# Performance work log

Measured on AMD Instinct MI355X. Metric: run time of the kernel, lower is better.

## Reference

```python
import jax, jax.numpy as jnp
import numpy as np

N = 50000          # nodes
E = 400000         # edges (before self loops)
F_IN = 128         # NUM_FEATURES
HID = 32           # hidden_dim
H = 12             # heads
HC = H * HID       # concat dim = 384
CLASSES = 40       # NUM_CLASSES
NEG_SLOPE = 0.2    # PyG GATv2 default


def setup_inputs() -> dict:
    key = jax.random.key(0)
    ks = jax.random.split(key, 16)

    def p(k, shape, fan_in):
        return (jax.random.normal(k, shape, jnp.float32) / np.sqrt(fan_in)).astype(jnp.float32)

    return {
        "x": jax.random.normal(ks[0], (N, F_IN), jnp.float32),
        "edge_index": jax.random.randint(ks[1], (2, E), 0, N, jnp.int32),
        # GATv2 layer 1 (share_weights=False)
        "Wl1": p(ks[2], (F_IN, HC), F_IN),
        "Wr1": p(ks[3], (F_IN, HC), F_IN),
        "a1": p(ks[4], (H, HID), HID),
        "b1": jnp.zeros((HC,), jnp.float32),
        # GATv2 layer 2
        "Wl2": p(ks[5], (HC, HC), HC),
        "Wr2": p(ks[6], (HC, HC), HC),
        "a2": p(ks[7], (H, HID), HID),
        "b2": jnp.zeros((HC,), jnp.float32),
        # MLP head
        "W3": p(ks[8], (HC, HID), HC),
        "b3": jnp.zeros((HID,), jnp.float32),
        "W4": p(ks[9], (HID, CLASSES), HID),
        "b4": jnp.zeros((CLASSES,), jnp.float32),
    }


def _gatv2(x, Wl, Wr, att, bias, src, dst):
    # source/target linear projections, per-head
    xl = (x @ Wl).reshape(-1, H, HID)   # [N,H,C] (message features)
    xr = (x @ Wr).reshape(-1, H, HID)   # [N,H,C]
    # per-edge attention logits: a^T LeakyReLU(xl_src + xr_dst)
    e = jax.nn.leaky_relu(xl[src] + xr[dst], NEG_SLOPE)   # [E',H,C]
    logit = jnp.einsum('ehc,hc->eh', e, att)              # [E',H]
    # segment softmax over incoming edges per dst node (self loops guarantee nonempty)
    m = jax.ops.segment_max(logit, dst, num_segments=N)   # [N,H]
    ex = jnp.exp(logit - m[dst])
    denom = jax.ops.segment_sum(ex, dst, num_segments=N)  # [N,H]
    alpha = ex / denom[dst]                                # [E',H]
    # weighted scatter-add of source messages
    out = jax.ops.segment_sum(xl[src] * alpha[:, :, None], dst, num_segments=N)
    return out.reshape(-1, HC) + bias


def reference(x, edge_index, Wl1, Wr1, a1, b1, Wl2, Wr2, a2, b2, W3, b3, W4, b4):
    # add_self_loops=True (PyG default)
    loops = jnp.arange(N, dtype=edge_index.dtype)
    src = jnp.concatenate([edge_index[0], loops])
    dst = jnp.concatenate([edge_index[1], loops])
    # dropout p=0.6 is identity in eval mode
    h = _gatv2(x, Wl1, Wr1, a1, b1, src, dst)
    h = jax.nn.elu(h)
    h = _gatv2(h, Wl2, Wr2, a2, b2, src, dst)
    h = jax.nn.elu(h)
    h = jax.nn.elu(h @ W3 + b3)
    h = h @ W4 + b4
    return jax.nn.log_softmax(h, axis=1)
```

## Files before the change

kernel.cpp:

```cpp
#include <hip/hip_runtime.h>
#include <hip/hip_bf16.h>
#include <math.h>

#define N_NODES 50000
#define E_EDGES 400000
#define EN_TOT  (E_EDGES + N_NODES)
#define F_IN    128
#define HC      384
#define CLASSES 40

typedef short short8 __attribute__((ext_vector_type(8)));
typedef float floatx4 __attribute__((ext_vector_type(4)));
typedef float floatx2 __attribute__((ext_vector_type(2)));
typedef unsigned int uint;

struct u3 { uint x, y, z; };

__device__ __forceinline__ float bf2f(unsigned short u) {
  union { unsigned int i; float f; } x; x.i = ((unsigned int)u) << 16; return x.f;
}
__device__ __forceinline__ unsigned short f2bf(float f) {
  union { float f; unsigned int i; } x; x.f = f;
  unsigned int r = x.i + 0x7fffu + ((x.i >> 16) & 1u);
  return (unsigned short)(r >> 16);
}
__device__ __forceinline__ float fin(float v) {
  return (fabsf(v) < 1e30f) ? v : 0.f;
}
__device__ __forceinline__ float rdw(const void* p, int idx, int fp32) {
  return fp32 ? ((const float*)p)[idx] : bf2f(((const unsigned short*)p)[idx]);
}

#if __has_builtin(__builtin_amdgcn_exp2f)
#define EXP2F(x) __builtin_amdgcn_exp2f(x)
#else
#define EXP2F(x) exp2f(x)
#endif

#if __has_builtin(__builtin_amdgcn_update_dpp)
#define DPP_ADD(w, ctrl) \
  (w += __int_as_float(__builtin_amdgcn_update_dpp(0, __float_as_int(w), ctrl, 0xf, 0xf, true)))
#define REDUCE16(w) do { DPP_ADD(w, 0xB1); DPP_ADD(w, 0x4E); DPP_ADD(w, 0x141); DPP_ADD(w, 0x140); } while (0)
#define DPP_MAXF(w, ctrl) do { float _t = __int_as_float(__builtin_amdgcn_update_dpp(0, \
    __float_as_int(w), ctrl, 0xf, 0xf, true)); w = fmaxf(w, _t); } while (0)
#define RED16MAX(w) do { DPP_MAXF(w, 0xB1); DPP_MAXF(w, 0x4E); DPP_MAXF(w, 0x141); DPP_MAXF(w, 0x140); } while (0)
#else
#define REDUCE16(w) do { w += __shfl_xor(w, 1); w += __shfl_xor(w, 2); \
                         w += __shfl_xor(w, 4); w += __shfl_xor(w, 8); } while (0)
#define RED16MAX(w) do { w = fmaxf(w, __shfl_xor(w, 1)); w = fmaxf(w, __shfl_xor(w, 2)); \
                         w = fmaxf(w, __shfl_xor(w, 4)); w = fmaxf(w, __shfl_xor(w, 8)); } while (0)
#endif


__global__ void k_sentinel(float* out, int n) {
  int i = blockIdx.x * 256 + threadIdx.x;
  if (i < n) out[i] = 111.0f;
}

__global__ void k_detect_zero(const unsigned short* __restrict__ x, int* __restrict__ flag,
                              int* __restrict__ counts, int* __restrict__ cursor) {
  int i = blockIdx.x * 256 + threadIdx.x;
  if (i < N_NODES) { counts[i] = 0; cursor[i] = 0; }
  if (blockIdx.x == 0 && threadIdx.x < 64) {
    int L = threadIdx.x;
    int sane = 0;
#pragma unroll
    for (int t = 0; t < 4; ++t) {
      unsigned short u = x[(size_t)(L * 4 + t) * 2];
      unsigned int mag = u & 0x7FFFu;
      unsigned int e   = (u >> 7) & 0xFFu;
      if (mag == 0u || (e >= 96u && e <= 159u)) sane++;
    }
    sane += __shfl_xor(sane, 1);
    sane += __shfl_xor(sane, 2);
    sane += __shfl_xor(sane, 4);
    sane += __shfl_xor(sane, 8);
    sane += __shfl_xor(sane, 16);
    sane += __shfl_xor(sane, 32);
    if (L == 0) flag[0] = (sane < 179) ? 1 : 0;
  }
}

__global__ void k_cvt(const void* __restrict__ x, unsigned short* __restrict__ Xb,
                      const int* __restrict__ flagp) {
  int i = blockIdx.x * 256 + threadIdx.x;
  if (i >= N_NODES * F_IN / 8) return;
  if (flagp[0]) {
    const floatx4* p = (const floatx4*)x + (size_t)i * 2;
    floatx4 f0 = p[0], f1 = p[1];
    short8 o;
#pragma unroll
    for (int j = 0; j < 4; ++j) { o[j] = (short)f2bf(f0[j]); o[4 + j] = (short)f2bf(f1[j]); }
    ((short8*)Xb)[i] = o;
  } else {
    ((short8*)Xb)[i] = ((const short8*)x)[i];
  }
}

__global__ void k_count(const int* __restrict__ ei, int* __restrict__ counts) {
  int e = blockIdx.x * 256 + threadIdx.x;
  if (e >= EN_TOT) return;
  int dst = (e < E_EDGES) ? ei[E_EDGES + e] : (e - E_EDGES);
  if ((unsigned)dst < N_NODES) atomicAdd(&counts[dst], 1);
}

__global__ void k_scan1(const int* __restrict__ counts, int* __restrict__ row_start,
                        int* __restrict__ bsum) {
  int b = blockIdx.x, tid = threadIdx.x;
  int i = b * 1024 + tid;
  int v = (i < N_NODES) ? counts[i] : 0;
  int lane = tid & 63, w = tid >> 6;
  int x = v;
#pragma unroll
  for (int d = 1; d < 64; d <<= 1) { int t = __shfl_up(x, d); if (lane >= d) x += t; }
  __shared__ int wsum[16];
  if (lane == 63) wsum[w] = x;
  __syncthreads();
  if (w == 0) {
    int y = (lane < 16) ? wsum[lane] : 0;
#pragma unroll
    for (int d = 1; d < 16; d <<= 1) { int t = __shfl_up(y, d); if (lane >= d) y += t; }
    if (lane < 16) wsum[lane] = y;
  }
  __syncthreads();
  if (w > 0) x += wsum[w - 1];
  if (i < N_NODES) row_start[i + 1] = x;
  if (tid == 1023) bsum[b] = x;
}

__global__ void k_scan23(int* __restrict__ row_start, const int* __restrict__ bsum, int nb) {
  int b = blockIdx.x, tid = threadIdx.x;
  __shared__ int sadd;
  if (tid < 64) {
    int lane = tid;
    int x = (lane < nb) ? bsum[lane] : 0;
#pragma unroll
    for (int d = 1; d < 64; d <<= 1) { int t = __shfl_up(x, d); if (lane >= d) x += t; }
    int pre = __shfl(x, (b > 0) ? (b - 1) : 0);
    if (tid == 0) sadd = (b > 0) ? pre : 0;
  }
  __syncthreads();
  int add = sadd;
  int i = b * 1024 + tid;
  if (i < N_NODES) row_start[i + 1] += add;
  if (i == 0) row_start[0] = 0;
}

__global__ void k_fill(const int* __restrict__ ei, const int* __restrict__ row_start,
                       int* __restrict__ cursor, int* __restrict__ csr_off) {
  int e = blockIdx.x * 256 + threadIdx.x;
  if (e >= EN_TOT) return;
  int src, dst;
  if (e < E_EDGES) { src = ei[e]; dst = ei[E_EDGES + e]; }
  else             { src = dst = e - E_EDGES; }
  if ((unsigned)dst >= N_NODES) return;
  int sv = ((unsigned)src < N_NODES) ? src : 0;
  int pos = atomicAdd(&cursor[dst], 1);
  int slot = row_start[dst] + pos;
  if ((unsigned)slot < EN_TOT) csr_off[slot] = sv * 768;
}

#define PK_J1 (F_IN * HC)
#define PK_J2 (2 * PK_J1)
#define PK_J3 (PK_J2 + HC * HC)
#define PK_J4 (PK_J3 + HC * HC)
#define PK_J5 (PK_J4 + HC * 32)
#define PK_J6 (PK_J5 + 32 * 48)
__global__ void k_pack_all(const void* __restrict__ Wl1, const void* __restrict__ Wr1,
                           const void* __restrict__ Wl2, const void* __restrict__ Wr2,
                           const void* __restrict__ W3, const void* __restrict__ W4,
                           unsigned short* __restrict__ BpL1, unsigned short* __restrict__ BpR1,
                           unsigned short* __restrict__ BpL2, unsigned short* __restrict__ BpR2,
                           unsigned short* __restrict__ Bp3, unsigned short* __restrict__ Bp4,
                           const int* __restrict__ flagp) {
  int gid = blockIdx.x * 256 + threadIdx.x;
  if (gid >= PK_J6) return;
  int fp32 = flagp[0];
  const void* src; unsigned short* dst; int NT, NCOL, idx;
  if (gid < PK_J2)      { NT = 24; NCOL = 384; if (gid < PK_J1) { src = Wl1; dst = BpL1; idx = gid; }
                                               else             { src = Wr1; dst = BpR1; idx = gid - PK_J1; } }
  else if (gid < PK_J4) { NT = 24; NCOL = 384; if (gid < PK_J3) { src = Wl2; dst = BpL2; idx = gid - PK_J2; }
                                               else             { src = Wr2; dst = BpR2; idx = gid - PK_J3; } }
  else if (gid < PK_J5) { NT = 2;  NCOL = 32;  src = W3; dst = Bp3; idx = gid - PK_J4; }
  else                  { NT = 3;  NCOL = 40;  src = W4; dst = Bp4; idx = gid - PK_J5; }
  int j  = idx & 7;
  int L  = (idx >> 3) & 63;
  int t  = idx >> 9;
  int nt = t % NT;
  int kt = t / NT;
  int k  = kt * 32 + ((L >> 4) * 8) + j;
  int n  = nt * 16 + (L & 15);
  float v = (n < NCOL) ? rdw(src, k * NCOL + n, fp32) : 0.f;
  dst[idx] = f2bf(fin(v));
}

#define LOADB(dst, kt) do { _Pragma("unroll") for (int n = 0; n < 6; ++n) \
    dst[n] = ((const short8*)Bp)[((size_t)((kt) * 24 + nt0 + n)) * 64 + lane]; } while (0)
#define DOMFMA(bf, kt) do { \
    short8 af[4]; \
    _Pragma("unroll") for (int mf = 0; mf < 4; ++mf) { \
      int row = mf * 16 + rsel; \
      int col = (kt) * 64 + kk16 * 16; \
      af[mf] = *(const short8*)(smem + row * RS + (col ^ ((row & 7) << 4))); } \
    _Pragma("unroll") for (int n = 0; n < 6; ++n) \
      _Pragma("unroll") for (int mf = 0; mf < 4; ++mf) \
        acc[mf][n] = __builtin_amdgcn_mfma_f32_16x16x32_bf16(af[mf], bf[n], acc[mf][n], 0, 0, 0); } while (0)

template<int NK>
__global__ __launch_bounds__(256, 2) void k_gemm2(const unsigned short* __restrict__ A_,
                       const unsigned short* __restrict__ BpL,
                       const unsigned short* __restrict__ BpR,
                       unsigned short* __restrict__ CL, unsigned short* __restrict__ CR) {
  constexpr int RS = NK * 64;
  __shared__ __align__(16) char smem[64 * 776];
  int which = blockIdx.x & 1;
  int bt    = blockIdx.x >> 1;
  const unsigned short* Bp = which ? BpR : BpL;
  unsigned short* C        = which ? CR  : CL;
  int tid  = threadIdx.x;
  int wave = tid >> 6, lane = tid & 63;
  int m0   = bt * 64;

  {
    uint4 v[NK];
#pragma unroll
    for (int i = 0; i < NK; ++i) {
      int o   = (i * 256 + tid) * 16;
      int row = o / RS;
      int rem = o - row * RS;
      int rg  = m0 + row; if (rg >= N_NODES) rg = N_NODES - 1;
      v[i] = *(const uint4*)((const char*)A_ + (size_t)rg * RS + rem);
    }
#pragma unroll
    for (int i = 0; i < NK; ++i) {
      int o   = (i * 256 + tid) * 16;
      int row = o / RS;
      int rem = o - row * RS;
      *(uint4*)(smem + row * RS + (rem ^ ((row & 7) << 4))) = v[i];
    }
  }

  int nt0  = wave * 6;
  int kk16 = (lane >> 4);
  int rsel = lane & 15;
  floatx4 acc[4][6];
#pragma unroll
  for (int mf = 0; mf < 4; ++mf)
#pragma unroll
    for (int n = 0; n < 6; ++n) acc[mf][n] = (floatx4){0.f, 0.f, 0.f, 0.f};

  short8 b0[6], b1[6], b2[6];
  LOADB(b0, 0);
  LOADB(b1, 1);
  __syncthreads();

#pragma unroll
  for (int kt = 0; kt < NK; ++kt) {
    if (kt + 2 < NK) {
      if (((kt + 2) % 3) == 0)      LOADB(b0, kt + 2);
      else if (((kt + 2) % 3) == 1) LOADB(b1, kt + 2);
      else                          LOADB(b2, kt + 2);
    }
    if ((kt % 3) == 0)      DOMFMA(b0, kt);
    else if ((kt % 3) == 1) DOMFMA(b1, kt);
    else                    DOMFMA(b2, kt);
  }

  __syncthreads();
  int qr = lane >> 4, ccol = lane & 15;
#pragma unroll
  for (int n = 0; n < 6; ++n) {
    int c    = (nt0 + n) * 16 + ccol;
    int soff = ((c & 127) >> 1) * 12 + (c >> 7) * 4 + (c & 1) * 2;
#pragma unroll
    for (int mf = 0; mf < 4; ++mf)
#pragma unroll
      for (int r = 0; r < 4; ++r) {
        int row = mf * 16 + qr * 4 + r;
        *(unsigned short*)(smem + row * 776 + soff) = f2bf(fin(acc[mf][n][r]));
      }
  }
  __syncthreads();
#pragma unroll
  for (int j = 0; j < 16; ++j) {
    int row = wave * 16 + j;
    int rg  = m0 + row;
    if (rg < N_NODES) {
      u3 val = *(const u3*)(smem + row * 776 + lane * 12);
      *(u3*)((char*)C + (size_t)rg * 768 + lane * 12) = val;
    }
  }
}

__global__ void k_edge(const unsigned short* __restrict__ XL, const unsigned short* __restrict__ XR,
                       const int* __restrict__ row_start, const int* __restrict__ csr_off,
                       const void* __restrict__ att, const void* __restrict__ bias,
                       unsigned short* __restrict__ H, const int* __restrict__ flagp) {
  int fp32 = flagp[0];
  int v = blockIdx.x;
  int L = threadIdx.x;
  int Lo = L * 12;
  floatx2 r2[3], a2[3];
  u3 rv3 = *(const u3*)((const char*)XR + (size_t)v * 768 + Lo);
  uint rr[3] = {rv3.x, rv3.y, rv3.z};
#pragma unroll
  for (int k = 0; k < 3; ++k) {
    r2[k].x = __uint_as_float(rr[k] << 16);
    r2[k].y = __uint_as_float(rr[k] & 0xffff0000u);
    int c = 2 * L + 128 * k;
    a2[k].x = fin(rdw(att, c,     fp32)) * 1.44269504088896f;
    a2[k].y = fin(rdw(att, c + 1, fp32)) * 1.44269504088896f;
  }
  float l[3] = {0.f, 0.f, 0.f};
  floatx2 acc[3];
#pragma unroll
  for (int k = 0; k < 3; ++k) acc[k] = (floatx2){0.f, 0.f};
  int beg = row_start[v], end = row_start[v + 1];
  if (beg < 0) beg = 0;
  if (end > EN_TOT) end = EN_TOT;
  const char* XLb = (const char*)XL;
  const unsigned OMAX = (N_NODES - 1) * 768u;
  for (int base = beg; base < end; base += 64) {
    int nE = end - base; if (nE > 64) nE = 64;
    int offv = (base + L < end) ? csr_off[base + L] : 0;
    int so = __builtin_amdgcn_readlane(offv, 0);
    if ((unsigned)so > OMAX) so = 0;
    u3 q = *(const u3*)(XLb + (unsigned)so + Lo);
    for (int j = 0; j < nE; ++j) {
      int sn = __builtin_amdgcn_readlane(offv, (j + 1) & 63);
      if ((unsigned)sn > OMAX) sn = 0;
      u3 qn = *(const u3*)(XLb + (unsigned)sn + Lo);
      uint qa[3] = {q.x, q.y, q.z};
#pragma unroll
      for (int k = 0; k < 3; ++k) {
        floatx2 sv;
        sv.x = __uint_as_float(qa[k] << 16);
        sv.y = __uint_as_float(qa[k] & 0xffff0000u);
        floatx2 t = sv + r2[k];
        t = __builtin_elementwise_max(t, t * 0.2f);
        floatx2 dw = t * a2[k];
        float w = dw.x + dw.y;
        REDUCE16(w);
        w = fminf(fmaxf(w, -126.f), 126.f);
        float p = EXP2F(w);
        l[k] += p;
        floatx2 pv = {p, p};
        acc[k] += pv * sv;
      }
      q = qn;
    }
  }
  uint* hr = (uint*)(H + (size_t)v * HC);
#pragma unroll
  for (int k = 0; k < 3; ++k) {
    int c = 2 * L + 128 * k;
    float inv = 1.f / fmaxf(l[k], 1e-30f);
    float o0 = acc[k].x * inv + fin(rdw(bias, c, fp32));
    float o1 = acc[k].y * inv + fin(rdw(bias, c + 1, fp32));
    o0 = o0 > 0.f ? o0 : expm1f(o0);
    o1 = o1 > 0.f ? o1 : expm1f(o1);
    hr[L + 64 * k] = (uint)f2bf(fin(o0)) | ((uint)f2bf(fin(o1)) << 16);
  }
}

__global__ void k_mlp(const unsigned short* __restrict__ H2,
                      const unsigned short* __restrict__ Bp3,
                      const unsigned short* __restrict__ Bp4,
                      const void* __restrict__ b3, const void* __restrict__ b4,
                      float* __restrict__ out, const int* __restrict__ flagp) {
  __shared__ float hs[16][33];
  int fp32 = flagp[0];
  int lane = threadIdx.x;
  int m0   = blockIdx.x * 16;
  int row  = m0 + (lane & 15);
  int kk   = (lane >> 4) * 8;
  floatx4 acc[2];
  acc[0] = (floatx4){0.f, 0.f, 0.f, 0.f};
  acc[1] = (floatx4){0.f, 0.f, 0.f, 0.f};
#pragma unroll
  for (int kt = 0; kt < 12; ++kt) {
    short8 af = *(const short8*)(H2 + (size_t)row * HC + kt * 32 + kk);
    const short8* bp = (const short8*)Bp3 + (size_t)kt * 2 * 64 + lane;
    acc[0] = __builtin_amdgcn_mfma_f32_16x16x32_bf16(af, bp[0],  acc[0], 0, 0, 0);
    acc[1] = __builtin_amdgcn_mfma_f32_16x16x32_bf16(af, bp[64], acc[1], 0, 0, 0);
  }
  int qr = lane >> 4, cc = lane & 15;
#pragma unroll
  for (int nt = 0; nt < 2; ++nt)
#pragma unroll
    for (int r = 0; r < 4; ++r) {
      int col = nt * 16 + cc;
      float s = acc[nt][r] + fin(rdw(b3, col, fp32));
      s = s > 0.f ? s : expm1f(s);
      hs[qr * 4 + r][col] = fin(s);
    }
  __syncthreads();
  short8 a2f;
#pragma unroll
  for (int j = 0; j < 8; ++j) a2f[j] = (short)f2bf(hs[lane & 15][kk + j]);
  floatx4 lg[3];
#pragma unroll
  for (int nt = 0; nt < 3; ++nt) {
    floatx4 z = (floatx4){0.f, 0.f, 0.f, 0.f};
    lg[nt] = __builtin_amdgcn_mfma_f32_16x16x32_bf16(a2f, ((const short8*)Bp4)[nt * 64 + lane], z, 0, 0, 0);
  }
  float bv[3];
#pragma unroll
  for (int nt = 0; nt < 3; ++nt) {
    int c = nt * 16 + cc;
    bv[nt] = (c < CLASSES) ? fin(rdw(b4, c, fp32)) : 0.f;
  }
#pragma unroll
  for (int r = 0; r < 4; ++r) {
    float v0 = lg[0][r] + bv[0];
    float v1 = lg[1][r] + bv[1];
    float v2 = (cc < 8) ? (lg[2][r] + bv[2]) : -1e30f;
    float mx = fmaxf(fmaxf(v0, v1), v2);
    RED16MAX(mx);
    float sm = __expf(v0 - mx) + __expf(v1 - mx) + ((cc < 8) ? __expf(v2 - mx) : 0.f);
    sm = (sm == sm) ? sm : 1.f;
    REDUCE16(sm);
    float ls = mx + logf(sm);
    float* op = out + (size_t)(m0 + qr * 4 + r) * CLASSES;
    op[cc]      = fin(v0 - ls);
    op[16 + cc] = fin(v1 - ls);
    if (cc < 8) op[32 + cc] = fin(v2 - ls);
  }
}

extern "C" void kernel_launch(void* const* d_in, const int* in_sizes, int n_in,
                              void* d_out, int out_size, void* d_ws, size_t ws_size,
                              hipStream_t stream) {
  const void* x   = d_in[0];
  const int* ei   = (const int*)d_in[1];
  const void* Wl1 = d_in[2];
  const void* Wr1 = d_in[3];
  const void* a1  = d_in[4];
  const void* b1  = d_in[5];
  const void* Wl2 = d_in[6];
  const void* Wr2 = d_in[7];
  const void* a2  = d_in[8];
  const void* b2  = d_in[9];
  const void* W3  = d_in[10];
  const void* b3  = d_in[11];
  const void* W4  = d_in[12];
  const void* b4  = d_in[13];
  float* out = (float*)d_out;

  char* ws = (char*)d_ws;
  size_t off = 0;
  auto alloc = [&](size_t bytes) { size_t o = off; off += (bytes + 255) & ~(size_t)255; return o; };
  int* flag       = (int*)(ws + alloc(256));
  int* row_start  = (int*)(ws + alloc((size_t)(N_NODES + 1) * 4));
  int* counts     = (int*)(ws + alloc((size_t)N_NODES * 4));
  int* cursor     = (int*)(ws + alloc((size_t)N_NODES * 4));
  int* bsum       = (int*)(ws + alloc(64 * 4));
  int* csr_off    = (int*)(ws + alloc((size_t)EN_TOT * 4));
  unsigned short* BpL1 = (unsigned short*)(ws + alloc((size_t)F_IN * HC * 2));
  unsigned short* BpR1 = (unsigned short*)(ws + alloc((size_t)F_IN * HC * 2));
  unsigned short* BpL2 = (unsigned short*)(ws + alloc((size_t)HC * HC * 2));
  unsigned short* BpR2 = (unsigned short*)(ws + alloc((size_t)HC * HC * 2));
  unsigned short* Bp3  = (unsigned short*)(ws + alloc((size_t)HC * 32 * 2));
  unsigned short* Bp4  = (unsigned short*)(ws + alloc((size_t)32 * 48 * 2));
  unsigned short* Xb   = (unsigned short*)(ws + alloc((size_t)N_NODES * F_IN * 2));
  unsigned short* B0   = (unsigned short*)(ws + alloc((size_t)N_NODES * HC * 2));
  unsigned short* B1   = (unsigned short*)(ws + alloc((size_t)N_NODES * HC * 2));
  unsigned short* B2   = (unsigned short*)(ws + alloc((size_t)N_NODES * HC * 2));
  (void)in_sizes; (void)n_in;

  if (ws_size < off) {
    k_sentinel<<<(out_size + 255) / 256, 256, 0, stream>>>(out, out_size);
    return;
  }

  const int SCAN_BLOCKS = (N_NODES + 1023) / 1024;
  const int GEMM_BLOCKS = 2 * ((N_NODES + 63) / 64);
  const int CVT_BLOCKS  = (N_NODES * F_IN / 8 + 255) / 256;

  k_detect_zero<<<(N_NODES + 255) / 256, 256, 0, stream>>>((const unsigned short*)x, flag, counts, cursor);
  k_cvt<<<CVT_BLOCKS, 256, 0, stream>>>(x, Xb, flag);
  k_count<<<(EN_TOT + 255) / 256, 256, 0, stream>>>(ei, counts);
  k_scan1<<<SCAN_BLOCKS, 1024, 0, stream>>>(counts, row_start, bsum);
  k_scan23<<<SCAN_BLOCKS, 1024, 0, stream>>>(row_start, bsum, SCAN_BLOCKS);
  k_fill<<<(EN_TOT + 255) / 256, 256, 0, stream>>>(ei, row_start, cursor, csr_off);

  k_pack_all<<<(PK_J6 + 255) / 256, 256, 0, stream>>>(Wl1, Wr1, Wl2, Wr2, W3, W4,
                                                      BpL1, BpR1, BpL2, BpR2, Bp3, Bp4, flag);

  k_gemm2<4><<<GEMM_BLOCKS, 256, 0, stream>>>(Xb, BpL1, BpR1, B0, B1);
  k_edge<<<N_NODES, 64, 0, stream>>>(B0, B1, row_start, csr_off, a1, b1, B1, flag);

  k_gemm2<12><<<GEMM_BLOCKS, 256, 0, stream>>>(B1, BpL2, BpR2, B2, B0);
  k_edge<<<N_NODES, 64, 0, stream>>>(B2, B0, row_start, csr_off, a2, b2, B1, flag);

  k_mlp<<<N_NODES / 16, 64, 0, stream>>>(B1, Bp3, Bp4, b3, b4, out, flag);
}
```

Measured before the change: 381.6 us.

## Prepack attention/bias params, deepen edge gather prefetch, shrink GEMM row tile

```diff
diff --git a/kernel.cpp b/kernel.cpp
--- a/kernel.cpp
+++ b/kernel.cpp
@@ -8,6 +8,7 @@
 #define F_IN    128
 #define HC      384
 #define CLASSES 40
+#define LOG2E   1.44269504088896f
 
 typedef short short8 __attribute__((ext_vector_type(8)));
 typedef float floatx4 __attribute__((ext_vector_type(4)));
@@ -166,16 +167,38 @@
 #define PK_J4 (PK_J3 + HC * HC)
 #define PK_J5 (PK_J4 + HC * 32)
 #define PK_J6 (PK_J5 + 32 * 48)
+#define PK_EX 3144
+#define PK_TOT (PK_J6 + PK_EX)
 __global__ void k_pack_all(const void* __restrict__ Wl1, const void* __restrict__ Wr1,
                            const void* __restrict__ Wl2, const void* __restrict__ Wr2,
                            const void* __restrict__ W3, const void* __restrict__ W4,
+                           const void* __restrict__ a1_, const void* __restrict__ a2_,
+                           const void* __restrict__ b1_, const void* __restrict__ b2_,
+                           const void* __restrict__ b3_, const void* __restrict__ b4_,
                            unsigned short* __restrict__ BpL1, unsigned short* __restrict__ BpR1,
                            unsigned short* __restrict__ BpL2, unsigned short* __restrict__ BpR2,
                            unsigned short* __restrict__ Bp3, unsigned short* __restrict__ Bp4,
+                           float* __restrict__ attp1, float* __restrict__ attp2,
+                           float* __restrict__ biasp1, float* __restrict__ biasp2,
+                           float* __restrict__ b3p, float* __restrict__ b4p,
                            const int* __restrict__ flagp) {
   int gid = blockIdx.x * 256 + threadIdx.x;
-  if (gid >= PK_J6) return;
+  if (gid >= PK_TOT) return;
   int fp32 = flagp[0];
+  if (gid >= PK_J6) {
+    int i = gid - PK_J6;
+    if (i < 3072) {
+      int seg = i / 768, r = i % 768;
+      int L = r / 6, q = r % 6, k = q >> 1, b = q & 1;
+      int c = 2 * L + 128 * k + b;
+      if (seg == 0)      attp1[r]  = fin(rdw(a1_, c, fp32)) * LOG2E;
+      else if (seg == 1) attp2[r]  = fin(rdw(a2_, c, fp32)) * LOG2E;
+      else if (seg == 2) biasp1[r] = fin(rdw(b1_, c, fp32));
+      else               biasp2[r] = fin(rdw(b2_, c, fp32));
+    } else if (i < 3104) b3p[i - 3072] = fin(rdw(b3_, i - 3072, fp32));
+    else                 b4p[i - 3104] = fin(rdw(b4_, i - 3104, fp32));
+    return;
+  }
   const void* src; unsigned short* dst; int NT, NCOL, idx;
   if (gid < PK_J2)      { NT = 24; NCOL = 384; if (gid < PK_J1) { src = Wl1; dst = BpL1; idx = gid; }
                                                else             { src = Wr1; dst = BpR1; idx = gid - PK_J1; } }
@@ -197,34 +220,35 @@
 #define LOADB(dst, kt) do { _Pragma("unroll") for (int n = 0; n < 6; ++n) \
     dst[n] = ((const short8*)Bp)[((size_t)((kt) * 24 + nt0 + n)) * 64 + lane]; } while (0)
 #define DOMFMA(bf, kt) do { \
-    short8 af[4]; \
-    _Pragma("unroll") for (int mf = 0; mf < 4; ++mf) { \
+    short8 af[2]; \
+    _Pragma("unroll") for (int mf = 0; mf < 2; ++mf) { \
       int row = mf * 16 + rsel; \
       int col = (kt) * 64 + kk16 * 16; \
       af[mf] = *(const short8*)(smem + row * RS + (col ^ ((row & 7) << 4))); } \
     _Pragma("unroll") for (int n = 0; n < 6; ++n) \
-      _Pragma("unroll") for (int mf = 0; mf < 4; ++mf) \
+      _Pragma("unroll") for (int mf = 0; mf < 2; ++mf) \
         acc[mf][n] = __builtin_amdgcn_mfma_f32_16x16x32_bf16(af[mf], bf[n], acc[mf][n], 0, 0, 0); } while (0)
 
 template<int NK>
-__global__ __launch_bounds__(256, 2) void k_gemm2(const unsigned short* __restrict__ A_,
+__global__ __launch_bounds__(256, 4) void k_gemm2(const unsigned short* __restrict__ A_,
                        const unsigned short* __restrict__ BpL,
                        const unsigned short* __restrict__ BpR,
                        unsigned short* __restrict__ CL, unsigned short* __restrict__ CR) {
-  constexpr int RS = NK * 64;
-  __shared__ __align__(16) char smem[64 * 776];
+  constexpr int RS  = NK * 64;
+  constexpr int NST = NK / 2;
+  __shared__ __align__(16) char smem[32 * 776];
   int which = blockIdx.x & 1;
   int bt    = blockIdx.x >> 1;
   const unsigned short* Bp = which ? BpR : BpL;
   unsigned short* C        = which ? CR  : CL;
   int tid  = threadIdx.x;
   int wave = tid >> 6, lane = tid & 63;
-  int m0   = bt * 64;
+  int m0   = bt * 32;
 
   {
-    uint4 v[NK];
-#pragma unroll
-    for (int i = 0; i < NK; ++i) {
+    uint4 v[NST];
+#pragma unroll
+    for (int i = 0; i < NST; ++i) {
       int o   = (i * 256 + tid) * 16;
       int row = o / RS;
       int rem = o - row * RS;
@@ -232,7 +256,7 @@
       v[i] = *(const uint4*)((const char*)A_ + (size_t)rg * RS + rem);
     }
 #pragma unroll
-    for (int i = 0; i < NK; ++i) {
+    for (int i = 0; i < NST; ++i) {
       int o   = (i * 256 + tid) * 16;
       int row = o / RS;
       int rem = o - row * RS;
@@ -243,9 +267,9 @@
   int nt0  = wave * 6;
   int kk16 = (lane >> 4);
   int rsel = lane & 15;
-  floatx4 acc[4][6];
-#pragma unroll
-  for (int mf = 0; mf < 4; ++mf)
+  floatx4 acc[2][6];
+#pragma unroll
+  for (int mf = 0; mf < 2; ++mf)
 #pragma unroll
     for (int n = 0; n < 6; ++n) acc[mf][n] = (floatx4){0.f, 0.f, 0.f, 0.f};
 
@@ -273,7 +297,7 @@
     int c    = (nt0 + n) * 16 + ccol;
     int soff = ((c & 127) >> 1) * 12 + (c >> 7) * 4 + (c & 1) * 2;
 #pragma unroll
-    for (int mf = 0; mf < 4; ++mf)
+    for (int mf = 0; mf < 2; ++mf)
 #pragma unroll
       for (int r = 0; r < 4; ++r) {
         int row = mf * 16 + qr * 4 + r;
@@ -282,8 +306,8 @@
   }
   __syncthreads();
 #pragma unroll
-  for (int j = 0; j < 16; ++j) {
-    int row = wave * 16 + j;
+  for (int j = 0; j < 8; ++j) {
+    int row = wave * 8 + j;
     int rg  = m0 + row;
     if (rg < N_NODES) {
       u3 val = *(const u3*)(smem + row * 776 + lane * 12);
@@ -292,24 +316,41 @@
   }
 }
 
+#define EBODY(q) do { \
+    uint _qa[3] = {(q).x, (q).y, (q).z}; \
+    _Pragma("unroll") \
+    for (int k = 0; k < 3; ++k) { \
+      floatx2 sv; \
+      sv.x = __uint_as_float(_qa[k] << 16); \
+      sv.y = __uint_as_float(_qa[k] & 0xffff0000u); \
+      floatx2 t = sv + r2[k]; \
+      t = __builtin_elementwise_max(t, t * 0.2f); \
+      floatx2 dw = t * a2[k]; \
+      float w = dw.x + dw.y; \
+      REDUCE16(w); \
+      w = fminf(fmaxf(w, -126.f), 126.f); \
+      float p = EXP2F(w); \
+      l[k] += p; \
+      floatx2 pv = {p, p}; \
+      acc[k] += pv * sv; \
+    } } while (0)
+
 __global__ void k_edge(const unsigned short* __restrict__ XL, const unsigned short* __restrict__ XR,
                        const int* __restrict__ row_start, const int* __restrict__ csr_off,
-                       const void* __restrict__ att, const void* __restrict__ bias,
-                       unsigned short* __restrict__ H, const int* __restrict__ flagp) {
-  int fp32 = flagp[0];
+                       const float* __restrict__ attp, const float* __restrict__ biasp,
+                       unsigned short* __restrict__ H) {
   int v = blockIdx.x;
   int L = threadIdx.x;
   int Lo = L * 12;
   floatx2 r2[3], a2[3];
   u3 rv3 = *(const u3*)((const char*)XR + (size_t)v * 768 + Lo);
   uint rr[3] = {rv3.x, rv3.y, rv3.z};
+  const floatx2* ap = (const floatx2*)(attp + L * 6);
 #pragma unroll
   for (int k = 0; k < 3; ++k) {
     r2[k].x = __uint_as_float(rr[k] << 16);
     r2[k].y = __uint_as_float(rr[k] & 0xffff0000u);
-    int c = 2 * L + 128 * k;
-    a2[k].x = fin(rdw(att, c,     fp32)) * 1.44269504088896f;
-    a2[k].y = fin(rdw(att, c + 1, fp32)) * 1.44269504088896f;
+    a2[k] = ap[k];
   }
   float l[3] = {0.f, 0.f, 0.f};
   floatx2 acc[3];
@@ -322,43 +363,34 @@
   const unsigned OMAX = (N_NODES - 1) * 768u;
   for (int base = beg; base < end; base += 64) {
     int nE = end - base; if (nE > 64) nE = 64;
+    int last = nE - 1;
     int offv = (base + L < end) ? csr_off[base + L] : 0;
-    int so = __builtin_amdgcn_readlane(offv, 0);
-    if ((unsigned)so > OMAX) so = 0;
-    u3 q = *(const u3*)(XLb + (unsigned)so + Lo);
-    for (int j = 0; j < nE; ++j) {
-      int sn = __builtin_amdgcn_readlane(offv, (j + 1) & 63);
-      if ((unsigned)sn > OMAX) sn = 0;
-      u3 qn = *(const u3*)(XLb + (unsigned)sn + Lo);
-      uint qa[3] = {q.x, q.y, q.z};
-#pragma unroll
-      for (int k = 0; k < 3; ++k) {
-        floatx2 sv;
-        sv.x = __uint_as_float(qa[k] << 16);
-        sv.y = __uint_as_float(qa[k] & 0xffff0000u);
-        floatx2 t = sv + r2[k];
-        t = __builtin_elementwise_max(t, t * 0.2f);
-        floatx2 dw = t * a2[k];
-        float w = dw.x + dw.y;
-        REDUCE16(w);
-        w = fminf(fmaxf(w, -126.f), 126.f);
-        float p = EXP2F(w);
-        l[k] += p;
-        floatx2 pv = {p, p};
-        acc[k] += pv * sv;
-      }
-      q = qn;
-    }
-  }
+#define RLD(i) ({ int _i = (i) > last ? last : (i); \
+                  int _s = __builtin_amdgcn_readlane(offv, _i); \
+                  if ((unsigned)_s > OMAX) _s = 0; \
+                  *(const u3*)(XLb + (unsigned)_s + Lo); })
+    u3 q0 = RLD(0), q1 = RLD(1), q2 = RLD(2), q3 = RLD(3);
+    int j = 0;
+    for (; j + 4 <= nE; j += 4) {
+      u3 n0 = RLD(j + 4), n1 = RLD(j + 5), n2 = RLD(j + 6), n3 = RLD(j + 7);
+      EBODY(q0); EBODY(q1); EBODY(q2); EBODY(q3);
+      q0 = n0; q1 = n1; q2 = n2; q3 = n3;
+    }
+    if (j < nE)     EBODY(q0);
+    if (j + 1 < nE) EBODY(q1);
+    if (j + 2 < nE) EBODY(q2);
+#undef RLD
+  }
+  const floatx2* bp = (const floatx2*)(biasp + L * 6);
   uint* hr = (uint*)(H + (size_t)v * HC);
 #pragma unroll
   for (int k = 0; k < 3; ++k) {
-    int c = 2 * L + 128 * k;
+    floatx2 bb = bp[k];
     float inv = 1.f / fmaxf(l[k], 1e-30f);
-    float o0 = acc[k].x * inv + fin(rdw(bias, c, fp32));
-    float o1 = acc[k].y * inv + fin(rdw(bias, c + 1, fp32));
-    o0 = o0 > 0.f ? o0 : expm1f(o0);
-    o1 = o1 > 0.f ? o1 : expm1f(o1);
+    float o0 = acc[k].x * inv + bb.x;
+    float o1 = acc[k].y * inv + bb.y;
+    o0 = o0 > 0.f ? o0 : EXP2F(o0 * LOG2E) - 1.f;
+    o1 = o1 > 0.f ? o1 : EXP2F(o1 * LOG2E) - 1.f;
     hr[L + 64 * k] = (uint)f2bf(fin(o0)) | ((uint)f2bf(fin(o1)) << 16);
   }
 }
@@ -366,10 +398,9 @@
 __global__ void k_mlp(const unsigned short* __restrict__ H2,
                       const unsigned short* __restrict__ Bp3,
                       const unsigned short* __restrict__ Bp4,
-                      const void* __restrict__ b3, const void* __restrict__ b4,
-                      float* __restrict__ out, const int* __restrict__ flagp) {
+                      const float* __restrict__ b3p, const float* __restrict__ b4p,
+                      float* __restrict__ out) {
   __shared__ float hs[16][33];
-  int fp32 = flagp[0];
   int lane = threadIdx.x;
   int m0   = blockIdx.x * 16;
   int row  = m0 + (lane & 15);
@@ -390,8 +421,8 @@
 #pragma unroll
     for (int r = 0; r < 4; ++r) {
       int col = nt * 16 + cc;
-      float s = acc[nt][r] + fin(rdw(b3, col, fp32));
-      s = s > 0.f ? s : expm1f(s);
+      float s = acc[nt][r] + b3p[col];
+      s = s > 0.f ? s : EXP2F(s * LOG2E) - 1.f;
       hs[qr * 4 + r][col] = fin(s);
     }
   __syncthreads();
@@ -408,7 +439,7 @@
 #pragma unroll
   for (int nt = 0; nt < 3; ++nt) {
     int c = nt * 16 + cc;
-    bv[nt] = (c < CLASSES) ? fin(rdw(b4, c, fp32)) : 0.f;
+    bv[nt] = (c < CLASSES) ? b4p[c] : 0.f;
   }
 #pragma unroll
   for (int r = 0; r < 4; ++r) {
@@ -462,6 +493,12 @@
   unsigned short* BpR2 = (unsigned short*)(ws + alloc((size_t)HC * HC * 2));
   unsigned short* Bp3  = (unsigned short*)(ws + alloc((size_t)HC * 32 * 2));
   unsigned short* Bp4  = (unsigned short*)(ws + alloc((size_t)32 * 48 * 2));
+  float* attp1  = (float*)(ws + alloc(768 * 4));
+  float* attp2  = (float*)(ws + alloc(768 * 4));
+  float* biasp1 = (float*)(ws + alloc(768 * 4));
+  float* biasp2 = (float*)(ws + alloc(768 * 4));
+  float* b3p    = (float*)(ws + alloc(32 * 4));
+  float* b4p    = (float*)(ws + alloc(40 * 4));
   unsigned short* Xb   = (unsigned short*)(ws + alloc((size_t)N_NODES * F_IN * 2));
   unsigned short* B0   = (unsigned short*)(ws + alloc((size_t)N_NODES * HC * 2));
   unsigned short* B1   = (unsigned short*)(ws + alloc((size_t)N_NODES * HC * 2));
@@ -474,7 +511,7 @@
   }
 
   const int SCAN_BLOCKS = (N_NODES + 1023) / 1024;
-  const int GEMM_BLOCKS = 2 * ((N_NODES + 63) / 64);
+  const int GEMM_BLOCKS = 2 * ((N_NODES + 31) / 32);
   const int CVT_BLOCKS  = (N_NODES * F_IN / 8 + 255) / 256;
 
   k_detect_zero<<<(N_NODES + 255) / 256, 256, 0, stream>>>((const unsigned short*)x, flag, counts, cursor);
@@ -484,14 +521,16 @@
   k_scan23<<<SCAN_BLOCKS, 1024, 0, stream>>>(row_start, bsum, SCAN_BLOCKS);
   k_fill<<<(EN_TOT + 255) / 256, 256, 0, stream>>>(ei, row_start, cursor, csr_off);
 
-  k_pack_all<<<(PK_J6 + 255) / 256, 256, 0, stream>>>(Wl1, Wr1, Wl2, Wr2, W3, W4,
-                                                      BpL1, BpR1, BpL2, BpR2, Bp3, Bp4, flag);
+  k_pack_all<<<(PK_TOT + 255) / 256, 256, 0, stream>>>(Wl1, Wr1, Wl2, Wr2, W3, W4,
+                                                       a1, a2, b1, b2, b3, b4,
+                                                       BpL1, BpR1, BpL2, BpR2, Bp3, Bp4,
+                                                       attp1, attp2, biasp1, biasp2, b3p, b4p, flag);
 
   k_gemm2<4><<<GEMM_BLOCKS, 256, 0, stream>>>(Xb, BpL1, BpR1, B0, B1);
-  k_edge<<<N_NODES, 64, 0, stream>>>(B0, B1, row_start, csr_off, a1, b1, B1, flag);
+  k_edge<<<N_NODES, 64, 0, stream>>>(B0, B1, row_start, csr_off, attp1, biasp1, B1);
 
   k_gemm2<12><<<GEMM_BLOCKS, 256, 0, stream>>>(B1, BpL2, BpR2, B2, B0);
-  k_edge<<<N_NODES, 64, 0, stream>>>(B2, B0, row_start, csr_off, a2, b2, B1, flag);
-
-  k_mlp<<<N_NODES / 16, 64, 0, stream>>>(B1, Bp3, Bp4, b3, b4, out, flag);
-}
+  k_edge<<<N_NODES, 64, 0, stream>>>(B2, B0, row_start, csr_off, attp2, biasp2, B1);
+
+  k_mlp<<<N_NODES / 16, 64, 0, stream>>>(B1, Bp3, Bp4, b3p, b4p, out);
+}
```

Result: faster. 351.0 us (-8.0%).
